# Kernel optimization log

Hardware: AMD Instinct MI355X
Metric: run time of the kernel (lower is better)

The kernel has to match this reference:

```python
import jax, jax.numpy as jnp
import numpy as np

N_MAX_L = (24, 20, 16, 12)   # basis size per angular channel l
N_SPECIES = 4
HIDDEN = 32
N_PAIRS = 1_500_000


def setup_inputs() -> dict:
    key = jax.random.key(0)
    ks = jax.random.split(key, 2 + 4 * len(N_MAX_L))
    inp = {
        "radial_functions": jax.random.normal(ks[0], (N_PAIRS, sum(N_MAX_L)), jnp.float32),
        "neighbor_species": jax.random.randint(ks[1], (N_PAIRS,), 0, N_SPECIES),
    }
    i = 2
    for l, n in enumerate(N_MAX_L):
        inp[f"w1_l{l}"] = jax.random.normal(ks[i], (N_SPECIES, n, HIDDEN), jnp.float32) * (n ** -0.5); i += 1
        inp[f"w2_l{l}"] = jax.random.normal(ks[i], (N_SPECIES, HIDDEN, HIDDEN), jnp.float32) * (HIDDEN ** -0.5); i += 1
        inp[f"w3_l{l}"] = jax.random.normal(ks[i], (N_SPECIES, HIDDEN, HIDDEN), jnp.float32) * (HIDDEN ** -0.5); i += 1
        inp[f"w4_l{l}"] = jax.random.normal(ks[i], (N_SPECIES, HIDDEN, n), jnp.float32) * (HIDDEN ** -0.5); i += 1
    return inp


def _species_mlp(x, neighbor_species, w1, w2, w3, w4):
    # x: [N, n_l]; weights: [S, ...]. For each row, apply the MLP of its species.
    # Equivalent to the torch gather -> tiny MLP -> scatter per species.
    out = jnp.zeros_like(x)
    for s in range(N_SPECIES):
        h = jax.nn.silu(x @ w1[s])
        h = jax.nn.silu(h @ w2[s])
        h = jax.nn.silu(h @ w3[s])
        y = h @ w4[s]
        out = jnp.where((neighbor_species == s)[:, None], y, out)
    return out


def reference(radial_functions, neighbor_species,
              w1_l0, w2_l0, w3_l0, w4_l0,
              w1_l1, w2_l1, w3_l1, w4_l1,
              w1_l2, w2_l2, w3_l2, w4_l2,
              w1_l3, w2_l3, w3_l3, w4_l3):
    ws = [(w1_l0, w2_l0, w3_l0, w4_l0),
          (w1_l1, w2_l1, w3_l1, w4_l1),
          (w1_l2, w2_l2, w3_l2, w4_l2),
          (w1_l3, w2_l3, w3_l3, w4_l3)]
    outs = []
    idx = 0
    for l, n in enumerate(N_MAX_L):
        x = radial_functions[:, idx:idx + n]
        idx += n
        outs.append(_species_mlp(x, neighbor_species, *ws[l]))
    # torch version returns a list of per-l blocks; we return them concatenated
    # along the feature axis ([N, sum(n_max_l)]) for a single-array output.
    return jnp.concatenate(outs, axis=1)
```

## Files before the change

### kernel.cpp

```cpp
#include <hip/hip_runtime.h>

typedef __attribute__((ext_vector_type(8))) short bf16x8;
typedef __attribute__((ext_vector_type(16))) float f32x16;

union FragU { bf16x8 v; unsigned int u[4]; };
struct Wptrs { const float* p[16]; };

#define ROWS 184
#define THREADS 512
#define SI 36

__device__ __forceinline__ unsigned int bfb(float f) {
  unsigned int u = __builtin_bit_cast(unsigned int, f);
  return (u + 0x7fffu + ((u >> 16) & 1u)) >> 16;
}
__device__ __forceinline__ unsigned int cvtpk(float lo, float hi) {
  unsigned int d;
  asm("v_cvt_pk_bf16_f32 %0, %1, %2" : "=v"(d) : "v"(lo), "v"(hi));
  return d;
}
__device__ __forceinline__ float bf2f(unsigned short b) {
  return __builtin_bit_cast(float, (unsigned int)b << 16);
}
__device__ __forceinline__ f32x16 zero16() {
  f32x16 z;
  #pragma unroll
  for (int i = 0; i < 16; ++i) z[i] = 0.0f;
  return z;
}
__device__ __forceinline__ bf16x8 ldA(const unsigned short* __restrict__ wsb, int tile, int l31, int hi, int h) {
  return *(const bf16x8*)(wsb + ((tile * 32 + l31) << 5) + h * 16 + hi * 8);
}

__device__ __forceinline__ void transition(const f32x16& acc, bf16x8& b0, bf16x8& b1) {
  unsigned int P[8];
  #pragma unroll
  for (int t = 0; t < 8; ++t) {
    float a0 = acc[2*t], a1 = acc[2*t+1];
    float d0 = 1.0f + __builtin_amdgcn_exp2f(a0);
    float d1 = 1.0f + __builtin_amdgcn_exp2f(a1);
    float r  = __builtin_amdgcn_rcpf(d0 * d1);
    float h0 = a0 * r * d1;
    float h1 = a1 * r * d0;
    P[t] = cvtpk(h0, h1);
  }
  asm volatile("v_permlane32_swap_b32 %0, %1" : "+v"(P[0]), "+v"(P[2]));
  asm volatile("v_permlane32_swap_b32 %0, %1" : "+v"(P[1]), "+v"(P[3]));
  asm volatile("v_permlane32_swap_b32 %0, %1" : "+v"(P[4]), "+v"(P[6]));
  asm volatile("v_permlane32_swap_b32 %0, %1" : "+v"(P[5]), "+v"(P[7]));
  FragU f0, f1;
  f0.u[0] = P[0]; f0.u[1] = P[1]; f0.u[2] = P[2]; f0.u[3] = P[3];
  f1.u[0] = P[4]; f1.u[1] = P[5]; f1.u[2] = P[6]; f1.u[3] = P[7];
  b0 = f0.v; b1 = f1.v;
}

template<int NL, int OFF, int TB>
__device__ __forceinline__ void phase(const float* __restrict__ rad,
    const unsigned short* __restrict__ wsb,
    unsigned short* s_in, unsigned short* s_out, const unsigned short* s_pos,
    const int* s_cnt, const int* s_off, const int* s_gpre,
    int base, int vb, int tid)
{
  constexpr int QPR = NL / 4;
  __syncthreads();
  for (int j = tid; j < vb * 8; j += THREADS) {
    int i = j >> 3, q = j & 7;
    uint2 w = make_uint2(0u, 0u);
    if (q < QPR) {
      float4 g = *(const float4*)(rad + (long)(base + i) * 72 + OFF + q * 4);
      w = make_uint2(cvtpk(g.x, g.y), cvtpk(g.z, g.w));
    }
    *(uint2*)(s_in + (int)s_pos[i] * SI + q * 4) = w;
  }
  __syncthreads();

  const int lane = tid & 63, wid = tid >> 6;
  const int l31 = lane & 31, hi = lane >> 5;
  const f32x16 Z = zero16();
  const int Gtot = s_gpre[4];
  for (int g = wid; g < Gtot; g += THREADS / 64) {
    int s = (g >= s_gpre[1]) + (g >= s_gpre[2]) + (g >= s_gpre[3]);
    int gi = g - s_gpre[s];
    int goff = s_off[s] + gi * 32;
    int gcnt = s_cnt[s] - gi * 32; if (gcnt > 32) gcnt = 32;
    int li = l31 < gcnt ? l31 : gcnt - 1;
    int row = goff + li;

    FragU bx0, bx1;
    bx0.v = *(const bf16x8*)(s_in + row * SI + hi * 8);
    if (NL > 16) bx1.v = *(const bf16x8*)(s_in + row * SI + 16 + hi * 8);

    f32x16 acc;
    acc = __builtin_amdgcn_mfma_f32_32x32x16_bf16(ldA(wsb, TB + s, l31, hi, 0), bx0.v, Z, 0, 0, 0);
    if (NL > 16)
      acc = __builtin_amdgcn_mfma_f32_32x32x16_bf16(ldA(wsb, TB + s, l31, hi, 1), bx1.v, acc, 0, 0, 0);
    bf16x8 b0, b1;
    transition(acc, b0, b1);
    acc = __builtin_amdgcn_mfma_f32_32x32x16_bf16(ldA(wsb, TB + 4 + s, l31, hi, 0), b0, Z, 0, 0, 0);
    acc = __builtin_amdgcn_mfma_f32_32x32x16_bf16(ldA(wsb, TB + 4 + s, l31, hi, 1), b1, acc, 0, 0, 0);
    transition(acc, b0, b1);
    acc = __builtin_amdgcn_mfma_f32_32x32x16_bf16(ldA(wsb, TB + 8 + s, l31, hi, 0), b0, Z, 0, 0, 0);
    acc = __builtin_amdgcn_mfma_f32_32x32x16_bf16(ldA(wsb, TB + 8 + s, l31, hi, 1), b1, acc, 0, 0, 0);
    transition(acc, b0, b1);
    acc = __builtin_amdgcn_mfma_f32_32x32x16_bf16(ldA(wsb, TB + 12 + s, l31, hi, 0), b0, Z, 0, 0, 0);
    acc = __builtin_amdgcn_mfma_f32_32x32x16_bf16(ldA(wsb, TB + 12 + s, l31, hi, 1), b1, acc, 0, 0, 0);

    if (l31 < gcnt) {
      int obase = (goff + l31) * 72 + OFF;
      #pragma unroll
      for (int t = 0; t < 4; ++t) {
        if (8 * t + 4 * hi + 4 <= NL) {
          *(uint2*)(s_out + obase + 8 * t + 4 * hi) =
              make_uint2(cvtpk(acc[4*t], acc[4*t+1]), cvtpk(acc[4*t+2], acc[4*t+3]));
        }
      }
    }
  }
}

__global__ void convert_weights_kernel(Wptrs wp, unsigned short* __restrict__ wsb) {
  int idx = blockIdx.x * 256 + threadIdx.x;
  const int NLs[4] = {24, 20, 16, 12};
  int l = idx >> 14, r = idx & 16383;
  int tile = r >> 10, j = (r >> 5) & 31, k = r & 31;
  int s = tile & 3, layer = tile >> 2;
  int NL = NLs[l];
  const float* w = wp.p[l * 4 + layer];
  float v = 0.0f;
  if (layer == 0)      { if (k < NL) v = w[(s * NL + k) * 32 + j] * -1.4426950408889634f; }
  else if (layer == 3) { if (j < NL) v = w[(s * 32 + k) * NL + j] * -0.6931471805599453f; }
  else                 { v = w[(s * 32 + k) * 32 + j]; }
  wsb[idx] = (unsigned short)bfb(v);
}

__global__ __launch_bounds__(THREADS, 8) void RadialBasis_51316269253437_kernel(
    const float* __restrict__ rad, const int* __restrict__ spc,
    const unsigned short* __restrict__ wsb, float* __restrict__ out, int npairs)
{
  __shared__ unsigned short s_in[ROWS * SI];
  __shared__ unsigned short s_out[ROWS * 72];
  __shared__ unsigned short s_pos[ROWS];
  __shared__ int s_cnt[4], s_fill[4], s_off[4], s_gpre[5];
  const int tid = threadIdx.x;
  const int base = blockIdx.x * ROWS;
  int vb = npairs - base; if (vb > ROWS) vb = ROWS;

  if (tid < 4) { s_cnt[tid] = 0; s_fill[tid] = 0; }
  __syncthreads();
  int sp = -1;
  if (tid < vb) sp = spc[base + tid];
  if (sp >= 0) atomicAdd(&s_cnt[sp], 1);
  __syncthreads();
  if (tid == 0) {
    int o = 0, gp = 0;
    #pragma unroll
    for (int s4 = 0; s4 < 4; ++s4) {
      s_off[s4] = o; o += s_cnt[s4];
      s_gpre[s4] = gp; gp += (s_cnt[s4] + 31) >> 5;
    }
    s_gpre[4] = gp;
  }
  __syncthreads();
  if (sp >= 0) {
    int pos = s_off[sp] + atomicAdd(&s_fill[sp], 1);
    s_pos[tid] = (unsigned short)pos;
  }
  phase<24,  0,  0>(rad, wsb, s_in, s_out, s_pos, s_cnt, s_off, s_gpre, base, vb, tid);
  phase<20, 24, 16>(rad, wsb, s_in, s_out, s_pos, s_cnt, s_off, s_gpre, base, vb, tid);
  phase<16, 44, 32>(rad, wsb, s_in, s_out, s_pos, s_cnt, s_off, s_gpre, base, vb, tid);
  phase<12, 60, 48>(rad, wsb, s_in, s_out, s_pos, s_cnt, s_off, s_gpre, base, vb, tid);
  __syncthreads();

  for (int j = tid; j < vb * 18; j += THREADS) {
    int i = j / 18, q = j - i * 18;
    uint2 w = *(const uint2*)(s_out + (int)s_pos[i] * 72 + q * 4);
    float4 v = make_float4(bf2f((unsigned short)(w.x & 0xffff)),
                           bf2f((unsigned short)(w.x >> 16)),
                           bf2f((unsigned short)(w.y & 0xffff)),
                           bf2f((unsigned short)(w.y >> 16)));
    *(float4*)(out + (long)(base + i) * 72 + q * 4) = v;
  }
}

extern "C" void kernel_launch(void* const* d_in, const int* in_sizes, int n_in,
                              void* d_out, int out_size, void* d_ws, size_t ws_size,
                              hipStream_t stream) {
  const float* rad = (const float*)d_in[0];
  const int* spc = (const int*)d_in[1];
  Wptrs wp;
  for (int i = 0; i < 16; ++i) wp.p[i] = (const float*)d_in[2 + i];
  float* out = (float*)d_out;
  unsigned short* wsb = (unsigned short*)d_ws;
  int npairs = in_sizes[0] / 72;

  convert_weights_kernel<<<dim3(256), dim3(256), 0, stream>>>(wp, wsb);
  int grid = (npairs + ROWS - 1) / ROWS;
  RadialBasis_51316269253437_kernel<<<dim3(grid), dim3(THREADS), 0, stream>>>(rad, spc, wsb, out, npairs);
}
```

Baseline: 316.1 us.

## Prefetch next channel's radial inputs into registers while computing current channel

Splits each per-channel phase into a register load stage and a compute stage. The global loads for channel l+1 are issued before channel l's MFMA chain runs, so their latency hides behind compute, and the converted values are written to LDS afterwards. Rows per block rise to 192 so the 3 fixed load slots per thread cover the tile, and the padded LDS row stride of 36 becomes 32, which may introduce bank conflicts. The change costs 12 extra VGPRs for the prefetch buffer, which may pressure the 8-waves-per-SIMD occupancy target.

```diff
diff --git a/kernel.cpp b/kernel.cpp
--- a/kernel.cpp
+++ b/kernel.cpp
@@ -6,9 +6,8 @@
 union FragU { bf16x8 v; unsigned int u[4]; };
 struct Wptrs { const float* p[16]; };
 
-#define ROWS 184
+#define ROWS 192
 #define THREADS 512
-#define SI 36
 
 __device__ __forceinline__ unsigned int bfb(float f) {
   unsigned int u = __builtin_bit_cast(unsigned int, f);
@@ -54,26 +53,37 @@
   b0 = f0.v; b1 = f1.v;
 }
 
+template<int NL, int OFF>
+__device__ __forceinline__ void load3(const float* __restrict__ rad,
+    int base, int vb, int tid, float4* L)
+{
+  #pragma unroll
+  for (int k = 0; k < 3; ++k) {
+    int j = tid + k * THREADS, i = j >> 3, q = j & 7;
+    float4 g = make_float4(0.f, 0.f, 0.f, 0.f);
+    if (q < NL / 4 && i < vb)
+      g = *(const float4*)(rad + (long)(base + i) * 72 + OFF + q * 4);
+    L[k] = g;
+  }
+}
+__device__ __forceinline__ void write3(unsigned short* __restrict__ s_in,
+    const unsigned short* __restrict__ s_pos, int vb, int tid, const float4* L)
+{
+  #pragma unroll
+  for (int k = 0; k < 3; ++k) {
+    int j = tid + k * THREADS, i = j >> 3, q = j & 7;
+    if (i < vb) {
+      *(uint2*)(s_in + (int)s_pos[i] * 32 + q * 4) =
+          make_uint2(cvtpk(L[k].x, L[k].y), cvtpk(L[k].z, L[k].w));
+    }
+  }
+}
+
 template<int NL, int OFF, int TB>
-__device__ __forceinline__ void phase(const float* __restrict__ rad,
-    const unsigned short* __restrict__ wsb,
-    unsigned short* s_in, unsigned short* s_out, const unsigned short* s_pos,
-    const int* s_cnt, const int* s_off, const int* s_gpre,
-    int base, int vb, int tid)
-{
-  constexpr int QPR = NL / 4;
-  __syncthreads();
-  for (int j = tid; j < vb * 8; j += THREADS) {
-    int i = j >> 3, q = j & 7;
-    uint2 w = make_uint2(0u, 0u);
-    if (q < QPR) {
-      float4 g = *(const float4*)(rad + (long)(base + i) * 72 + OFF + q * 4);
-      w = make_uint2(cvtpk(g.x, g.y), cvtpk(g.z, g.w));
-    }
-    *(uint2*)(s_in + (int)s_pos[i] * SI + q * 4) = w;
-  }
-  __syncthreads();
-
+__device__ __forceinline__ void computePhase(const unsigned short* __restrict__ wsb,
+    const unsigned short* __restrict__ s_in, unsigned short* __restrict__ s_out,
+    const int* s_cnt, const int* s_off, const int* s_gpre, int tid)
+{
   const int lane = tid & 63, wid = tid >> 6;
   const int l31 = lane & 31, hi = lane >> 5;
   const f32x16 Z = zero16();
@@ -87,8 +97,8 @@
     int row = goff + li;
 
     FragU bx0, bx1;
-    bx0.v = *(const bf16x8*)(s_in + row * SI + hi * 8);
-    if (NL > 16) bx1.v = *(const bf16x8*)(s_in + row * SI + 16 + hi * 8);
+    bx0.v = *(const bf16x8*)(s_in + row * 32 + hi * 8);
+    if (NL > 16) bx1.v = *(const bf16x8*)(s_in + row * 32 + 16 + hi * 8);
 
     f32x16 acc;
     acc = __builtin_amdgcn_mfma_f32_32x32x16_bf16(ldA(wsb, TB + s, l31, hi, 0), bx0.v, Z, 0, 0, 0);
@@ -137,7 +147,7 @@
     const float* __restrict__ rad, const int* __restrict__ spc,
     const unsigned short* __restrict__ wsb, float* __restrict__ out, int npairs)
 {
-  __shared__ unsigned short s_in[ROWS * SI];
+  __shared__ unsigned short s_in[ROWS * 32];
   __shared__ unsigned short s_out[ROWS * 72];
   __shared__ unsigned short s_pos[ROWS];
   __shared__ int s_cnt[4], s_fill[4], s_off[4], s_gpre[5];
@@ -165,10 +175,32 @@
     int pos = s_off[sp] + atomicAdd(&s_fill[sp], 1);
     s_pos[tid] = (unsigned short)pos;
   }
-  phase<24,  0,  0>(rad, wsb, s_in, s_out, s_pos, s_cnt, s_off, s_gpre, base, vb, tid);
-  phase<20, 24, 16>(rad, wsb, s_in, s_out, s_pos, s_cnt, s_off, s_gpre, base, vb, tid);
-  phase<16, 44, 32>(rad, wsb, s_in, s_out, s_pos, s_cnt, s_off, s_gpre, base, vb, tid);
-  phase<12, 60, 48>(rad, wsb, s_in, s_out, s_pos, s_cnt, s_off, s_gpre, base, vb, tid);
+
+  float4 L[3];
+  load3<24, 0>(rad, base, vb, tid, L);
+  __syncthreads();
+  write3(s_in, s_pos, vb, tid, L);
+  __syncthreads();
+
+  load3<20, 24>(rad, base, vb, tid, L);
+  computePhase<24,  0,  0>(wsb, s_in, s_out, s_cnt, s_off, s_gpre, tid);
+  __syncthreads();
+  write3(s_in, s_pos, vb, tid, L);
+  __syncthreads();
+
+  load3<16, 44>(rad, base, vb, tid, L);
+  computePhase<20, 24, 16>(wsb, s_in, s_out, s_cnt, s_off, s_gpre, tid);
+  __syncthreads();
+  write3(s_in, s_pos, vb, tid, L);
+  __syncthreads();
+
+  load3<12, 60>(rad, base, vb, tid, L);
+  computePhase<16, 44, 32>(wsb, s_in, s_out, s_cnt, s_off, s_gpre, tid);
+  __syncthreads();
+  write3(s_in, s_pos, vb, tid, L);
+  __syncthreads();
+
+  computePhase<12, 60, 48>(wsb, s_in, s_out, s_cnt, s_off, s_gpre, tid);
   __syncthreads();
 
   for (int j = tid; j < vb * 18; j += THREADS) {
```

Result: slower. 354.8 us (+12.2%).

## Load MLP inputs directly from global memory via an inverse permutation, dropping LDS staging

Applied to the files above, without the earlier changes.

Removes the per-phase LDS staging buffer for the input features, along with its two barriers per phase. Each lane now gathers its row's radial values straight from global memory using an inverse permutation array (s_perm) and converts them to bf16 in registers. Freeing that LDS allows a larger row tile per block (ROWS raised from 184 to 192). The trade-off is scattered, less coalesced global reads issued inside the MFMA loop, and the loads may be less able to overlap with compute.

```diff
diff --git a/kernel.cpp b/kernel.cpp
--- a/kernel.cpp
+++ b/kernel.cpp
@@ -6,9 +6,8 @@
 union FragU { bf16x8 v; unsigned int u[4]; };
 struct Wptrs { const float* p[16]; };
 
-#define ROWS 184
+#define ROWS 192
 #define THREADS 512
-#define SI 36
 
 __device__ __forceinline__ unsigned int bfb(float f) {
   unsigned int u = __builtin_bit_cast(unsigned int, f);
@@ -55,25 +54,12 @@
 }
 
 template<int NL, int OFF, int TB>
-__device__ __forceinline__ void phase(const float* __restrict__ rad,
-    const unsigned short* __restrict__ wsb,
-    unsigned short* s_in, unsigned short* s_out, const unsigned short* s_pos,
+__device__ __forceinline__ void phaseDirect(const float* __restrict__ rad,
+    const unsigned short* __restrict__ wsb, unsigned short* __restrict__ s_out,
+    const unsigned short* __restrict__ s_perm,
     const int* s_cnt, const int* s_off, const int* s_gpre,
-    int base, int vb, int tid)
+    int base, int tid)
 {
-  constexpr int QPR = NL / 4;
-  __syncthreads();
-  for (int j = tid; j < vb * 8; j += THREADS) {
-    int i = j >> 3, q = j & 7;
-    uint2 w = make_uint2(0u, 0u);
-    if (q < QPR) {
-      float4 g = *(const float4*)(rad + (long)(base + i) * 72 + OFF + q * 4);
-      w = make_uint2(cvtpk(g.x, g.y), cvtpk(g.z, g.w));
-    }
-    *(uint2*)(s_in + (int)s_pos[i] * SI + q * 4) = w;
-  }
-  __syncthreads();
-
   const int lane = tid & 63, wid = tid >> 6;
   const int l31 = lane & 31, hi = lane >> 5;
   const f32x16 Z = zero16();
@@ -84,11 +70,25 @@
     int goff = s_off[s] + gi * 32;
     int gcnt = s_cnt[s] - gi * 32; if (gcnt > 32) gcnt = 32;
     int li = l31 < gcnt ? l31 : gcnt - 1;
-    int row = goff + li;
+    const float* rp = rad + (long)(base + (int)s_perm[goff + li]) * 72 + OFF;
 
     FragU bx0, bx1;
-    bx0.v = *(const bf16x8*)(s_in + row * SI + hi * 8);
-    if (NL > 16) bx1.v = *(const bf16x8*)(s_in + row * SI + 16 + hi * 8);
+    {
+      int kl = hi * 8;
+      float4 q0 = make_float4(0.f,0.f,0.f,0.f), q1 = q0;
+      if (kl + 4 <= NL) q0 = *(const float4*)(rp + kl);
+      if (kl + 8 <= NL) q1 = *(const float4*)(rp + kl + 4);
+      bx0.u[0] = cvtpk(q0.x, q0.y); bx0.u[1] = cvtpk(q0.z, q0.w);
+      bx0.u[2] = cvtpk(q1.x, q1.y); bx0.u[3] = cvtpk(q1.z, q1.w);
+      if (NL > 16) {
+        int k2 = 16 + hi * 8;
+        float4 r0 = make_float4(0.f,0.f,0.f,0.f), r1 = r0;
+        if (k2 + 4 <= NL) r0 = *(const float4*)(rp + k2);
+        if (k2 + 8 <= NL) r1 = *(const float4*)(rp + k2 + 4);
+        bx1.u[0] = cvtpk(r0.x, r0.y); bx1.u[1] = cvtpk(r0.z, r0.w);
+        bx1.u[2] = cvtpk(r1.x, r1.y); bx1.u[3] = cvtpk(r1.z, r1.w);
+      }
+    }
 
     f32x16 acc;
     acc = __builtin_amdgcn_mfma_f32_32x32x16_bf16(ldA(wsb, TB + s, l31, hi, 0), bx0.v, Z, 0, 0, 0);
@@ -137,9 +137,9 @@
     const float* __restrict__ rad, const int* __restrict__ spc,
     const unsigned short* __restrict__ wsb, float* __restrict__ out, int npairs)
 {
-  __shared__ unsigned short s_in[ROWS * SI];
   __shared__ unsigned short s_out[ROWS * 72];
   __shared__ unsigned short s_pos[ROWS];
+  __shared__ unsigned short s_perm[ROWS];
   __shared__ int s_cnt[4], s_fill[4], s_off[4], s_gpre[5];
   const int tid = threadIdx.x;
   const int base = blockIdx.x * ROWS;
@@ -164,11 +164,14 @@
   if (sp >= 0) {
     int pos = s_off[sp] + atomicAdd(&s_fill[sp], 1);
     s_pos[tid] = (unsigned short)pos;
-  }
-  phase<24,  0,  0>(rad, wsb, s_in, s_out, s_pos, s_cnt, s_off, s_gpre, base, vb, tid);
-  phase<20, 24, 16>(rad, wsb, s_in, s_out, s_pos, s_cnt, s_off, s_gpre, base, vb, tid);
-  phase<16, 44, 32>(rad, wsb, s_in, s_out, s_pos, s_cnt, s_off, s_gpre, base, vb, tid);
-  phase<12, 60, 48>(rad, wsb, s_in, s_out, s_pos, s_cnt, s_off, s_gpre, base, vb, tid);
+    s_perm[pos] = (unsigned short)tid;
+  }
+  __syncthreads();
+
+  phaseDirect<24,  0,  0>(rad, wsb, s_out, s_perm, s_cnt, s_off, s_gpre, base, tid);
+  phaseDirect<20, 24, 16>(rad, wsb, s_out, s_perm, s_cnt, s_off, s_gpre, base, tid);
+  phaseDirect<16, 44, 32>(rad, wsb, s_out, s_perm, s_cnt, s_off, s_gpre, base, tid);
+  phaseDirect<12, 60, 48>(rad, wsb, s_out, s_perm, s_cnt, s_off, s_gpre, base, tid);
   __syncthreads();
 
   for (int j = tid; j < vb * 18; j += THREADS) {
```

Result: slower. 330.6 us (+4.6%).
